# Kernel tuning notes

Hardware: AMD Instinct MI355X
Metric: run time of the kernel (lower is better)

## Reference

```python
import jax, jax.numpy as jnp
import numpy as np

N_NODES = 20000
N_EDGES = 320000
HIDDEN = 64
HEADS = 8
HEAD_DIM = HIDDEN // HEADS
K_HOPS = 2
CST = 1e-05


def setup_inputs() -> dict:
    key = jax.random.key(0)
    ks = jax.random.split(key, 12)
    s = 1.0 / np.sqrt(HIDDEN)
    inp = {
        "x": jax.random.normal(ks[0], (N_NODES, HIDDEN), dtype=jnp.float32),
        "edge_index": jax.random.randint(ks[1], (2, N_EDGES), 0, N_NODES, dtype=jnp.int64),
        "edge_feature": jnp.zeros((1,), dtype=jnp.float32),  # unused by the module
        "Wq": jax.random.uniform(ks[2], (HIDDEN, HIDDEN), jnp.float32, -s, s),
        "bq": jax.random.uniform(ks[3], (HIDDEN,), jnp.float32, -s, s),
        "Wk": jax.random.uniform(ks[4], (HIDDEN, HIDDEN), jnp.float32, -s, s),
        "bk": jax.random.uniform(ks[5], (HIDDEN,), jnp.float32, -s, s),
        "Wv": jax.random.uniform(ks[6], (HIDDEN, HIDDEN), jnp.float32, -s, s),
        "bv": jax.random.uniform(ks[7], (HIDDEN,), jnp.float32, -s, s),
        "Wo": jax.random.uniform(ks[8], (HIDDEN, HIDDEN), jnp.float32, -s, s),
        "bo": jax.random.uniform(ks[9], (HIDDEN,), jnp.float32, -s, s),
        "hopwise": jnp.ones((K_HOPS + 1,), dtype=jnp.float32),
        "headwise": jnp.zeros((HEADS, K_HOPS), dtype=jnp.float32),
    }
    return inp


def reference(x, edge_index, edge_feature, Wq, bq, Wk, bk, Wv, bv, Wo, bo, hopwise, headwise):
    N = x.shape[0]
    row, col = edge_index[0], edge_index[1]

    # symmetric normalization: deg is in-degree of col
    deg = jax.ops.segment_sum(jnp.ones_like(col, dtype=x.dtype), col, num_segments=N)
    deg_inv = jnp.where(deg > 0, deg ** -0.5, 0.0)
    norm = deg_inv[row] * deg_inv[col]  # [E]

    Q = 1.0 + jax.nn.elu(x @ Wq + bq)
    K = 1.0 + jax.nn.elu(x @ Wk + bk)
    V = (x @ Wv + bv)
    Q = Q.reshape(N, HEADS, HEAD_DIM)
    K = K.reshape(N, HEADS, HEAD_DIM)
    V = V.reshape(N, HEADS, HEAD_DIM)

    M = jnp.einsum('nhi,nhj->nhij', K, V)  # [N,H,d,d]
    hidden = V * hopwise[0]
    layerwise = jax.nn.softmax(headwise, axis=0)  # softmax over heads (dim=-2)

    for hop in range(K_HOPS):
        # scatter-add propagation: out[i] = sum_{e: col[e]=i} norm[e] * state[row[e]]
        M = jax.ops.segment_sum(norm[:, None, None, None] * M[row], col, num_segments=N)
        K = jax.ops.segment_sum(norm[:, None, None] * K[row], col, num_segments=N)
        H = jnp.einsum('nhi,nhij->nhj', Q, M)
        C = jnp.einsum('nhi,nhi->nh', Q, K)[..., None] + CST
        H = H / C
        gamma = hopwise[hop + 1] * layerwise[:, hop][:, None]  # [H,1]
        hidden = hidden + gamma * H

    hidden = hidden.reshape(N, HEADS * HEAD_DIM)
    # dropout is identity in eval mode
    return hidden @ Wo + bo
```

## Files before the change

### kernel.cpp

```cpp
#include <hip/hip_runtime.h>
#include <hip/hip_bf16.h>

typedef __hip_bfloat16 bf16;
typedef __fp16 half2_t __attribute__((ext_vector_type(2)));
typedef float floatx2 __attribute__((ext_vector_type(2)));

#define N_NODES 20000
#define N_EDGES 320000
#define CSTF 1e-5f

#if defined(__has_builtin)
#if __has_builtin(__builtin_amdgcn_cvt_pk_fp8_f32) && __has_builtin(__builtin_amdgcn_cvt_pk_f32_fp8)
#define M1FP8 1
#endif
#if __has_builtin(__builtin_amdgcn_fdot2)
#define HAVE_FDOT2 1
#endif
#endif

#ifdef M1FP8
#define M1_STRIDE 128
#define M1_LANE   2
typedef uint2 m1vec;
#else
#define M1_STRIDE 256
#define M1_LANE   4
typedef uint4 m1vec;
#endif

__device__ __forceinline__ half2_t u2h(unsigned int u) {
    union { unsigned int u; half2_t h; } c; c.u = u; return c.h;
}
__device__ __forceinline__ unsigned int pkh(float a, float b) {
    union { __fp16 h[2]; unsigned int u; } c;
    c.h[0] = (__fp16)a; c.h[1] = (__fp16)b;
    return c.u;
}
__device__ __forceinline__ float fdot2(half2_t a, half2_t b, float c) {
#ifdef HAVE_FDOT2
    return __builtin_amdgcn_fdot2(a, b, c, false);
#else
    return fmaf((float)a.x, (float)b.x, fmaf((float)a.y, (float)b.y, c));
#endif
}
__device__ __forceinline__ int rdl(int v, int lane) { return __builtin_amdgcn_readlane(v, lane); }
__device__ __forceinline__ float ldf(const void* p, int i, bool bf) {
    return bf ? __bfloat162float(((const bf16*)p)[i]) : ((const float*)p)[i];
}
__device__ __forceinline__ bool wave_is_i64(const void* ei, int e) {
    unsigned int hi = ((const unsigned int*)ei)[2 * e + 1];
    return !__any(hi != 0);
}

struct Args {
    const void *x, *ei, *Wq, *bq, *Wk, *bk, *Wv, *bv, *Wo, *bo, *hopwise, *headwise;
    void* out;
    float* Q;
    _Float16 *K0h, *Vh, *K1h;
    unsigned int* M1h;
    int* bsrc;
    float* gbuf;
    int *deg, *cnt;
};

__global__ __launch_bounds__(256) void k_p1(Args a) {
    const int t = threadIdx.x;
    const int e = blockIdx.x * 256 + t;
    bool i64 = wave_is_i64(a.ei, e);
    int r, c;
    if (i64) {
        r = (int)((const long long*)a.ei)[e];
        c = (int)((const long long*)a.ei)[N_EDGES + e];
    } else {
        r = ((const int*)a.ei)[e];
        c = ((const int*)a.ei)[N_EDGES + e];
    }
    int slot = atomicAdd(&a.deg[c], 1);
    if (slot < 64) a.bsrc[c * 64 + slot] = r;
    if (blockIdx.x < 64) {
        int bad = 0;
        for (int i = blockIdx.x * 256 + t; i < 40000; i += 64 * 256) {
            unsigned int w = ((const unsigned int*)a.x)[i];
            if (((w >> 7)  & 0xFFu) == 0xFFu) bad++;
            if (((w >> 23) & 0xFFu) == 0xFFu) bad++;
        }
        if (bad) atomicAdd(&a.cnt[0], bad);
    }
}

__global__ __launch_bounds__(256) void k_p2(Args a) {
    __shared__ __fp16 sWh[3 * 4096];
    __shared__ float sx[8][64];
    const int t = threadIdx.x;
    const bool bf = (a.cnt[0] < 16);
    const int n0 = blockIdx.x * 8;
    for (int i = t; i < 4096; i += 256) {
        int k = i >> 6, col = i & 63;
        int di_ = (k >> 1) * 128 + col * 2 + (k & 1);
        sWh[di_]        = (__fp16)ldf(a.Wq, i, bf);
        sWh[4096 + di_] = (__fp16)ldf(a.Wk, i, bf);
        sWh[8192 + di_] = (__fp16)ldf(a.Wv, i, bf);
    }
    for (int i = t; i < 512; i += 256) {
        int row = i >> 6, col = i & 63;
        sx[row][col] = ldf(a.x, (n0 + row) * 64 + col, bf);
    }
    if (blockIdx.x == 0 && t < 8) {
        float e0 = 0.0f, e1 = 0.0f;
        for (int hh = 0; hh < 8; hh++) {
            e0 += __expf(ldf(a.headwise, hh * 2 + 0, bf));
            e1 += __expf(ldf(a.headwise, hh * 2 + 1, bf));
        }
        float hw1 = ldf(a.hopwise, 1, bf), hw2 = ldf(a.hopwise, 2, bf);
        a.gbuf[t]     = hw1 * __expf(ldf(a.headwise, t * 2 + 0, bf)) / e0;
        a.gbuf[8 + t] = hw2 * __expf(ldf(a.headwise, t * 2 + 1, bf)) / e1;
        if (t == 0) a.gbuf[16] = ldf(a.hopwise, 0, bf);
    }
    __syncthreads();
    const unsigned int* sWq = (const unsigned int*)sWh;
    const unsigned int* sWk = sWq + 2048;
    const unsigned int* sWv = sWq + 4096;
    const int l = t & 63, sub = t >> 6;
    const float bqv = ldf(a.bq, l, bf), bkv = ldf(a.bk, l, bf), bvv = ldf(a.bv, l, bf);
    for (int g = 0; g < 2; g++) {
        int row = g * 4 + sub;
        int n = n0 + row;
        float q = bqv, k = bkv, v = bvv;
        const float2* xp = (const float2*)sx[row];
#pragma unroll 8
        for (int kp = 0; kp < 32; kp++) {
            float2 xv = xp[kp];
            half2_t xh = u2h(pkh(xv.x, xv.y));
            q = fdot2(xh, u2h(sWq[kp * 64 + l]), q);
            k = fdot2(xh, u2h(sWk[kp * 64 + l]), k);
            v = fdot2(xh, u2h(sWv[kp * 64 + l]), v);
        }
        int dg = a.deg[n];
        float di = dg > 0 ? rsqrtf((float)dg) : 0.0f;
        a.Q[n * 64 + l] = q > 0.0f ? q + 1.0f : __expf(q);
        float kel = k > 0.0f ? k + 1.0f : __expf(k);
        a.K0h[n * 64 + l] = (_Float16)(di * kel);
        a.Vh[n * 64 + l]  = (_Float16)v;
    }
}

__global__ __launch_bounds__(128) void k_hop1(Args a) {
    const int l = threadIdx.x & 63;
    const int n = blockIdx.x * 2 + (threadIdx.x >> 6);
    const int hb = l & 56;
    float acc[8] = {0, 0, 0, 0, 0, 0, 0, 0};
    float kacc = 0.0f;
    const int dg = a.deg[n];
    const int m = min(dg, 64);
    if (m > 0) {
        const int srcv = a.bsrc[n * 64 + (l < m ? l : m - 1)];
#define H1_ACC(KU, VO, KO)                                                 \
    {                                                                      \
        half2_t p0 = u2h(KU.x), p1 = u2h(KU.y), p2 = u2h(KU.z), p3 = u2h(KU.w); \
        float vv = (float)VO;                                              \
        acc[0] = fmaf(vv, (float)p0.x, acc[0]); acc[1] = fmaf(vv, (float)p0.y, acc[1]); \
        acc[2] = fmaf(vv, (float)p1.x, acc[2]); acc[3] = fmaf(vv, (float)p1.y, acc[3]); \
        acc[4] = fmaf(vv, (float)p2.x, acc[4]); acc[5] = fmaf(vv, (float)p2.y, acc[5]); \
        acc[6] = fmaf(vv, (float)p3.x, acc[6]); acc[7] = fmaf(vv, (float)p3.y, acc[7]); \
        kacc += (float)KO;                                                 \
    }
        int e = 0;
        for (; e + 8 <= m; e += 8) {
            int s_[8];
            uint4 k_[8];
            __fp16 v_[8], o_[8];
#pragma unroll
            for (int u = 0; u < 8; u++) s_[u] = rdl(srcv, e + u);
#pragma unroll
            for (int u = 0; u < 8; u++) k_[u] = *(const uint4*)(a.K0h + s_[u] * 64 + hb);
#pragma unroll
            for (int u = 0; u < 8; u++) v_[u] = a.Vh[s_[u] * 64 + l];
#pragma unroll
            for (int u = 0; u < 8; u++) o_[u] = a.K0h[s_[u] * 64 + l];
#pragma unroll
            for (int u = 0; u < 8; u++) H1_ACC(k_[u], v_[u], o_[u])
        }
        for (; e < m; e++) {
            int sA = rdl(srcv, e);
            uint4 kA = *(const uint4*)(a.K0h + sA * 64 + hb);
            __fp16 vA = a.Vh[sA * 64 + l];
            __fp16 oA = a.K0h[sA * 64 + l];
            H1_ACC(kA, vA, oA)
        }
#undef H1_ACC
        float inv = 1.0f / (float)dg;
#pragma unroll
        for (int i = 0; i < 8; i++) acc[i] *= inv;
        kacc *= inv;
    }
#ifdef M1FP8
    unsigned int w0 = 0, w1 = 0;
    w0 = __builtin_amdgcn_cvt_pk_fp8_f32(acc[0], acc[1], w0, false);
    w0 = __builtin_amdgcn_cvt_pk_fp8_f32(acc[2], acc[3], w0, true);
    w1 = __builtin_amdgcn_cvt_pk_fp8_f32(acc[4], acc[5], w1, false);
    w1 = __builtin_amdgcn_cvt_pk_fp8_f32(acc[6], acc[7], w1, true);
    uint2 o2; o2.x = w0; o2.y = w1;
    *(uint2*)(a.M1h + (size_t)n * M1_STRIDE + l * M1_LANE) = o2;
#else
    uint4 o;
    o.x = pkh(acc[0], acc[1]); o.y = pkh(acc[2], acc[3]);
    o.z = pkh(acc[4], acc[5]); o.w = pkh(acc[6], acc[7]);
    *(uint4*)(a.M1h + (size_t)n * M1_STRIDE + l * M1_LANE) = o;
#endif
    a.K1h[n * 64 + l] = (_Float16)kacc;
}

__global__ __launch_bounds__(128) void k_hop2f(Args a) {
    const bool bf = (a.cnt[0] < 16);
    const int t = threadIdx.x;
    const int l = t & 63;
    const int n = blockIdx.x * 2 + (t >> 6);
    const int hb = l & 56, h = l >> 3;
    const float4 qa = *(const float4*)(a.Q + n * 64 + hb);
    const float4 qb = *(const float4*)(a.Q + n * 64 + hb + 4);
    const float qown = a.Q[n * 64 + l];
    const int dg = a.deg[n];
    const int m = min(dg, 64);
    floatx2 s01 = {0, 0}, s23 = {0, 0}, s45 = {0, 0}, s67 = {0, 0};
    float sk = 0.0f;

#ifdef M1FP8
#define H2_ACC(MU, KO)                                                     \
    {                                                                      \
        s01 += __builtin_amdgcn_cvt_pk_f32_fp8(MU.x, false);               \
        s23 += __builtin_amdgcn_cvt_pk_f32_fp8(MU.x, true);                \
        s45 += __builtin_amdgcn_cvt_pk_f32_fp8(MU.y, false);               \
        s67 += __builtin_amdgcn_cvt_pk_f32_fp8(MU.y, true);                \
        sk += (float)KO;                                                   \
    }
#define H2_DOT(MU, DST)                                                    \
    {                                                                      \
        floatx2 a0 = __builtin_amdgcn_cvt_pk_f32_fp8(MU.x, false);         \
        floatx2 a1 = __builtin_amdgcn_cvt_pk_f32_fp8(MU.x, true);          \
        floatx2 a2 = __builtin_amdgcn_cvt_pk_f32_fp8(MU.y, false);         \
        floatx2 a3 = __builtin_amdgcn_cvt_pk_f32_fp8(MU.y, true);          \
        DST = qa.x * a0.x;                                                 \
        DST = fmaf(qa.y, a0.y, DST); DST = fmaf(qa.z, a1.x, DST);          \
        DST = fmaf(qa.w, a1.y, DST); DST = fmaf(qb.x, a2.x, DST);          \
        DST = fmaf(qb.y, a2.y, DST); DST = fmaf(qb.z, a3.x, DST);          \
        DST = fmaf(qb.w, a3.y, DST);                                       \
    }
#else
    const half2_t one2 = u2h(pkh(1.0f, 1.0f));
#define H2_ACC(MU, KO)                                                     \
    {                                                                      \
        half2_t p0 = u2h(MU.x), p1 = u2h(MU.y), p2 = u2h(MU.z), p3 = u2h(MU.w); \
        s01.x += (float)p0.x; s01.y += (float)p0.y;                        \
        s23.x += (float)p1.x; s23.y += (float)p1.y;                        \
        s45.x += (float)p2.x; s45.y += (float)p2.y;                        \
        s67.x += (float)p3.x; s67.y += (float)p3.y;                        \
        sk += (float)KO;                                                   \
    }
    const half2_t q01 = u2h(pkh(qa.x, qa.y));
    const half2_t q23 = u2h(pkh(qa.z, qa.w));
    const half2_t q45 = u2h(pkh(qb.x, qb.y));
    const half2_t q67 = u2h(pkh(qb.z, qb.w));
#define H2_DOT(MU, DST)                                                    \
    {                                                                      \
        DST = fdot2(q01, u2h(MU.x), 0.0f);                                 \
        DST = fdot2(q23, u2h(MU.y), DST);                                  \
        DST = fdot2(q45, u2h(MU.z), DST);                                  \
        DST = fdot2(q67, u2h(MU.w), DST);                                  \
    }
#endif

    if (m > 0) {
        const int srcv = a.bsrc[n * 64 + (l < m ? l : m - 1)];
        int e = 0;
        for (; e + 8 <= m; e += 8) {
            int s_[8];
            m1vec m_[8];
            __fp16 k_[8];
#pragma unroll
            for (int u = 0; u < 8; u++) s_[u] = rdl(srcv, e + u);
#pragma unroll
            for (int u = 0; u < 8; u++) m_[u] = *(const m1vec*)(a.M1h + (size_t)s_[u] * M1_STRIDE + l * M1_LANE);
#pragma unroll
            for (int u = 0; u < 8; u++) k_[u] = a.K1h[s_[u] * 64 + l];
#pragma unroll
            for (int u = 0; u < 8; u++) H2_ACC(m_[u], k_[u])
        }
        for (; e < m; e++) {
            int sA = rdl(srcv, e);
            m1vec mA = *(const m1vec*)(a.M1h + (size_t)sA * M1_STRIDE + l * M1_LANE);
            __fp16 kA = a.K1h[sA * 64 + l];
            H2_ACC(mA, kA)
        }
    }
#undef H2_ACC
    float hacc = qa.x * s01.x;
    hacc = fmaf(qa.y, s01.y, hacc); hacc = fmaf(qa.z, s23.x, hacc);
    hacc = fmaf(qa.w, s23.y, hacc); hacc = fmaf(qb.x, s45.x, hacc);
    hacc = fmaf(qb.y, s45.y, hacc); hacc = fmaf(qb.z, s67.x, hacc);
    hacc = fmaf(qb.w, s67.y, hacc);
    m1vec mo = *(const m1vec*)(a.M1h + (size_t)n * M1_STRIDE + l * M1_LANE);
    float h1r;
    H2_DOT(mo, h1r)
#undef H2_DOT
    const float din = dg > 0 ? rsqrtf((float)dg) : 0.0f;
    const float sq  = dg > 0 ? sqrtf((float)dg)  : 0.0f;
    float h1 = h1r * sq;
    float c1 = qown * (float)a.K1h[n * 64 + l];
    float c2 = qown * sk;
#pragma unroll
    for (int dd = 1; dd < 8; dd <<= 1) {
        c1 += __shfl_xor(c1, dd);
        c2 += __shfl_xor(c2, dd);
    }
    c1 *= sq;
    c2 *= din;
    float H2v = hacc * din;

    const float hw0 = a.gbuf[16];
    const float g1 = a.gbuf[h];
    const float g2 = a.gbuf[8 + h];
    float hidden = hw0 * (float)a.Vh[n * 64 + l] + g1 * h1 / (c1 + CSTF) + g2 * H2v / (c2 + CSTF);

    float o = ldf(a.bo, l, bf);
#pragma unroll 16
    for (int k = 0; k < 64; k++) {
        float hk = __shfl(hidden, k);
        o += hk * ldf(a.Wo, k * 64 + l, bf);
    }
    if (bf) ((bf16*)a.out)[n * 64 + l] = __float2bfloat16(o);
    else    ((float*)a.out)[n * 64 + l] = o;
}

extern "C" void kernel_launch(void* const* d_in, const int* in_sizes, int n_in,
                              void* d_out, int out_size, void* d_ws, size_t ws_size,
                              hipStream_t stream) {
    char* p = (char*)d_ws;
    auto alloc = [&](size_t bytes) {
        void* r = (void*)p;
        p += (bytes + 255) & ~(size_t)255;
        return r;
    };
    Args a;
    a.x = d_in[0];  a.ei = d_in[1];
    a.Wq = d_in[3]; a.bq = d_in[4];
    a.Wk = d_in[5]; a.bk = d_in[6];
    a.Wv = d_in[7]; a.bv = d_in[8];
    a.Wo = d_in[9]; a.bo = d_in[10];
    a.hopwise = d_in[11]; a.headwise = d_in[12];
    a.out = d_out;

    a.Q    = (float*)alloc((size_t)N_NODES * 64 * 4);
    a.K0h  = (_Float16*)alloc((size_t)N_NODES * 64 * 2);
    a.Vh   = (_Float16*)alloc((size_t)N_NODES * 64 * 2);
    a.K1h  = (_Float16*)alloc((size_t)N_NODES * 64 * 2);
    a.M1h  = (unsigned int*)alloc((size_t)N_NODES * 1024);
    a.bsrc = (int*)alloc((size_t)N_NODES * 64 * 4);
    a.gbuf = (float*)alloc(32 * 4);
    int* zz = (int*)alloc(((size_t)N_NODES + 64) * 4);
    a.deg = zz;
    a.cnt = zz + N_NODES;

    (void)hipMemsetAsync(zz, 0, ((size_t)N_NODES + 64) * 4, stream);

    const int EB = (N_EDGES + 255) / 256;
    k_p1<<<EB, 256, 0, stream>>>(a);
    k_p2<<<2500, 256, 0, stream>>>(a);
    k_hop1<<<N_NODES / 2, 128, 0, stream>>>(a);
    k_hop2f<<<N_NODES / 2, 128, 0, stream>>>(a);
}
```

Baseline: 194.3 us.

## Fuse edge bucketing and QKV projection into one launch, defer degree scaling

Merges the edge-bucketing/degree-count kernel and the QKV projection kernel into a single launch. QKV blocks and edge blocks run concurrently, which removes one kernel boundary. Because the degree is not final when K is computed, the source-degree normalisation moves into hop1 as a per-edge rsqrt of deg[src]. The bf16 detection in the QKV blocks now samples the weight matrices locally instead of reading the global counter. Hop kernels also go from 128 to 256 threads per block, and hop1 takes on extra gathered degree loads.

```diff
diff --git a/kernel.cpp b/kernel.cpp
--- a/kernel.cpp
+++ b/kernel.cpp
@@ -44,6 +44,9 @@
 #endif
 }
 __device__ __forceinline__ int rdl(int v, int lane) { return __builtin_amdgcn_readlane(v, lane); }
+__device__ __forceinline__ float rdlf(float v, int lane) {
+    return __int_as_float(__builtin_amdgcn_readlane(__float_as_int(v), lane));
+}
 __device__ __forceinline__ float ldf(const void* p, int i, bool bf) {
     return bf ? __bfloat162float(((const bf16*)p)[i]) : ((const float*)p)[i];
 }
@@ -63,36 +66,55 @@
     int *deg, *cnt;
 };
 
-__global__ __launch_bounds__(256) void k_p1(Args a) {
-    const int t = threadIdx.x;
-    const int e = blockIdx.x * 256 + t;
-    bool i64 = wave_is_i64(a.ei, e);
-    int r, c;
-    if (i64) {
-        r = (int)((const long long*)a.ei)[e];
-        c = (int)((const long long*)a.ei)[N_EDGES + e];
-    } else {
-        r = ((const int*)a.ei)[e];
-        c = ((const int*)a.ei)[N_EDGES + e];
-    }
-    int slot = atomicAdd(&a.deg[c], 1);
-    if (slot < 64) a.bsrc[c * 64 + slot] = r;
-    if (blockIdx.x < 64) {
-        int bad = 0;
-        for (int i = blockIdx.x * 256 + t; i < 40000; i += 64 * 256) {
-            unsigned int w = ((const unsigned int*)a.x)[i];
-            if (((w >> 7)  & 0xFFu) == 0xFFu) bad++;
-            if (((w >> 23) & 0xFFu) == 0xFFu) bad++;
-        }
-        if (bad) atomicAdd(&a.cnt[0], bad);
-    }
-}
-
-__global__ __launch_bounds__(256) void k_p2(Args a) {
+#define QKV_BLOCKS 2500
+__global__ __launch_bounds__(256) void k_p12(Args a) {
     __shared__ __fp16 sWh[3 * 4096];
     __shared__ float sx[8][64];
+    __shared__ int sbad;
     const int t = threadIdx.x;
-    const bool bf = (a.cnt[0] < 16);
+    if (blockIdx.x >= QKV_BLOCKS) {
+        const int e = (blockIdx.x - QKV_BLOCKS) * 256 + t;
+        bool i64 = wave_is_i64(a.ei, e);
+        int r, c;
+        if (i64) {
+            r = (int)((const long long*)a.ei)[e];
+            c = (int)((const long long*)a.ei)[N_EDGES + e];
+        } else {
+            r = ((const int*)a.ei)[e];
+            c = ((const int*)a.ei)[N_EDGES + e];
+        }
+        int slot = atomicAdd(&a.deg[c], 1);
+        if (slot < 64) a.bsrc[c * 64 + slot] = r;
+        if (blockIdx.x < QKV_BLOCKS + 64) {
+            int bad = 0;
+            for (int i = (blockIdx.x - QKV_BLOCKS) * 256 + t; i < 40000; i += 64 * 256) {
+                unsigned int w = ((const unsigned int*)a.x)[i];
+                if (((w >> 7)  & 0xFFu) == 0xFFu) bad++;
+                if (((w >> 23) & 0xFFu) == 0xFFu) bad++;
+            }
+            if (bad) atomicAdd(&a.cnt[0], bad);
+        }
+        return;
+    }
+    if (t == 0) sbad = 0;
+    __syncthreads();
+    {
+        int bad = 0;
+        for (int i = t; i < 2048; i += 256) {
+            unsigned int wq = ((const unsigned int*)a.Wq)[i];
+            unsigned int wk = ((const unsigned int*)a.Wk)[i];
+            unsigned int wv = ((const unsigned int*)a.Wv)[i];
+            if (((wq >> 7)  & 0xFFu) == 0xFFu) bad++;
+            if (((wq >> 23) & 0xFFu) == 0xFFu) bad++;
+            if (((wk >> 7)  & 0xFFu) == 0xFFu) bad++;
+            if (((wk >> 23) & 0xFFu) == 0xFFu) bad++;
+            if (((wv >> 7)  & 0xFFu) == 0xFFu) bad++;
+            if (((wv >> 23) & 0xFFu) == 0xFFu) bad++;
+        }
+        if (bad) atomicAdd(&sbad, bad);
+    }
+    __syncthreads();
+    const bool bf = (sbad < 2);
     const int n0 = blockIdx.x * 8;
     for (int i = t; i < 4096; i += 256) {
         int k = i >> 6, col = i & 63;
@@ -135,18 +157,15 @@
             k = fdot2(xh, u2h(sWk[kp * 64 + l]), k);
             v = fdot2(xh, u2h(sWv[kp * 64 + l]), v);
         }
-        int dg = a.deg[n];
-        float di = dg > 0 ? rsqrtf((float)dg) : 0.0f;
         a.Q[n * 64 + l] = q > 0.0f ? q + 1.0f : __expf(q);
-        float kel = k > 0.0f ? k + 1.0f : __expf(k);
-        a.K0h[n * 64 + l] = (_Float16)(di * kel);
+        a.K0h[n * 64 + l] = (_Float16)(k > 0.0f ? k + 1.0f : __expf(k));
         a.Vh[n * 64 + l]  = (_Float16)v;
     }
 }
 
-__global__ __launch_bounds__(128) void k_hop1(Args a) {
+__global__ __launch_bounds__(256) void k_hop1(Args a) {
     const int l = threadIdx.x & 63;
-    const int n = blockIdx.x * 2 + (threadIdx.x >> 6);
+    const int n = blockIdx.x * 4 + (threadIdx.x >> 6);
     const int hb = l & 56;
     float acc[8] = {0, 0, 0, 0, 0, 0, 0, 0};
     float kacc = 0.0f;
@@ -154,21 +173,22 @@
     const int m = min(dg, 64);
     if (m > 0) {
         const int srcv = a.bsrc[n * 64 + (l < m ? l : m - 1)];
-#define H1_ACC(KU, VO, KO)                                                 \
+#define H1_ACC(KU, VO, KO, DI)                                             \
     {                                                                      \
         half2_t p0 = u2h(KU.x), p1 = u2h(KU.y), p2 = u2h(KU.z), p3 = u2h(KU.w); \
-        float vv = (float)VO;                                              \
+        float vv = DI * (float)VO;                                         \
         acc[0] = fmaf(vv, (float)p0.x, acc[0]); acc[1] = fmaf(vv, (float)p0.y, acc[1]); \
         acc[2] = fmaf(vv, (float)p1.x, acc[2]); acc[3] = fmaf(vv, (float)p1.y, acc[3]); \
         acc[4] = fmaf(vv, (float)p2.x, acc[4]); acc[5] = fmaf(vv, (float)p2.y, acc[5]); \
         acc[6] = fmaf(vv, (float)p3.x, acc[6]); acc[7] = fmaf(vv, (float)p3.y, acc[7]); \
-        kacc += (float)KO;                                                 \
+        kacc = fmaf(DI, (float)KO, kacc);                                  \
     }
         int e = 0;
         for (; e + 8 <= m; e += 8) {
             int s_[8];
             uint4 k_[8];
             __fp16 v_[8], o_[8];
+            float d_[8];
 #pragma unroll
             for (int u = 0; u < 8; u++) s_[u] = rdl(srcv, e + u);
 #pragma unroll
@@ -178,14 +198,17 @@
 #pragma unroll
             for (int u = 0; u < 8; u++) o_[u] = a.K0h[s_[u] * 64 + l];
 #pragma unroll
-            for (int u = 0; u < 8; u++) H1_ACC(k_[u], v_[u], o_[u])
+            for (int u = 0; u < 8; u++) d_[u] = rsqrtf((float)a.deg[s_[u]]);
+#pragma unroll
+            for (int u = 0; u < 8; u++) H1_ACC(k_[u], v_[u], o_[u], d_[u])
         }
         for (; e < m; e++) {
             int sA = rdl(srcv, e);
             uint4 kA = *(const uint4*)(a.K0h + sA * 64 + hb);
             __fp16 vA = a.Vh[sA * 64 + l];
             __fp16 oA = a.K0h[sA * 64 + l];
-            H1_ACC(kA, vA, oA)
+            float dA = rsqrtf((float)a.deg[sA]);
+            H1_ACC(kA, vA, oA, dA)
         }
 #undef H1_ACC
         float inv = 1.0f / (float)dg;
@@ -210,11 +233,11 @@
     a.K1h[n * 64 + l] = (_Float16)kacc;
 }
 
-__global__ __launch_bounds__(128) void k_hop2f(Args a) {
+__global__ __launch_bounds__(256) void k_hop2f(Args a) {
     const bool bf = (a.cnt[0] < 16);
     const int t = threadIdx.x;
     const int l = t & 63;
-    const int n = blockIdx.x * 2 + (t >> 6);
+    const int n = blockIdx.x * 4 + (t >> 6);
     const int hb = l & 56, h = l >> 3;
     const float4 qa = *(const float4*)(a.Q + n * 64 + hb);
     const float4 qb = *(const float4*)(a.Q + n * 64 + hb + 4);
@@ -246,7 +269,6 @@
         DST = fmaf(qb.w, a3.y, DST);                                       \
     }
 #else
-    const half2_t one2 = u2h(pkh(1.0f, 1.0f));
 #define H2_ACC(MU, KO)                                                     \
     {                                                                      \
         half2_t p0 = u2h(MU.x), p1 = u2h(MU.y), p2 = u2h(MU.z), p3 = u2h(MU.w); \
@@ -363,8 +385,7 @@
     (void)hipMemsetAsync(zz, 0, ((size_t)N_NODES + 64) * 4, stream);
 
     const int EB = (N_EDGES + 255) / 256;
-    k_p1<<<EB, 256, 0, stream>>>(a);
-    k_p2<<<2500, 256, 0, stream>>>(a);
-    k_hop1<<<N_NODES / 2, 128, 0, stream>>>(a);
-    k_hop2f<<<N_NODES / 2, 128, 0, stream>>>(a);
-}
+    k_p12<<<QKV_BLOCKS + EB, 256, 0, stream>>>(a);
+    k_hop1<<<N_NODES / 4, 256, 0, stream>>>(a);
+    k_hop2f<<<N_NODES / 4, 256, 0, stream>>>(a);
+}
```

Measured after the change: 198.7 us. 1.02x slower.
